# Performance work log

Hardware: AMD Instinct MI355X
Metric: run time of the kernel (lower is better)

Reference implementation:

```python
import math
import jax, jax.numpy as jnp
import numpy as np

B, S, D_MODEL = 4, 2048, 1024
N_HEADS, D_KV = 16, 64
INNER = N_HEADS * D_KV
NUM_BUCKETS = 32
MAX_DISTANCE = 128


def _relative_position_bucket(relative_position, bidirectional=True,
                              num_buckets=32, max_distance=128):
    # Faithful port of T5Attention._relative_position_bucket
    ret = jnp.zeros_like(relative_position)
    n = -relative_position
    if bidirectional:
        num_buckets //= 2
        ret = ret + (n < 0).astype(jnp.int32) * num_buckets
        n = jnp.abs(n)
    else:
        n = jnp.maximum(n, 0)
    max_exact = num_buckets // 2
    is_small = n < max_exact
    # safe log: n>=max_exact wherever this branch is selected
    val_if_large = max_exact + (
        jnp.log(jnp.maximum(n, 1).astype(jnp.float32) / max_exact)
        / math.log(max_distance / max_exact) * (num_buckets - max_exact)
    ).astype(jnp.int32)
    val_if_large = jnp.minimum(val_if_large, num_buckets - 1)
    return ret + jnp.where(is_small, n, val_if_large)


def setup_inputs() -> dict:
    key = jax.random.key(0)
    k_h, k_q, k_k, k_v, k_o, k_e = jax.random.split(key, 6)
    std = D_MODEL ** -0.5
    return {
        "hidden_states": jax.random.normal(k_h, (B, S, D_MODEL), dtype=jnp.float32),
        "Wq": jax.random.normal(k_q, (D_MODEL, INNER), dtype=jnp.float32) * std,
        "Wk": jax.random.normal(k_k, (D_MODEL, INNER), dtype=jnp.float32) * std,
        "Wv": jax.random.normal(k_v, (D_MODEL, INNER), dtype=jnp.float32) * std,
        "Wo": jax.random.normal(k_o, (INNER, D_MODEL), dtype=jnp.float32) * std,
        "rel_emb": jax.random.normal(k_e, (NUM_BUCKETS, N_HEADS), dtype=jnp.float32) * std,
    }


def reference(hidden_states, Wq, Wk, Wv, Wo, rel_emb):
    b, s, _ = hidden_states.shape
    # QKV projections (T5: no bias, no 1/sqrt(d) scaling of scores)
    def shape_heads(x):  # [b, s, inner] -> [b, h, s, d_kv]
        return x.reshape(b, s, N_HEADS, D_KV).transpose(0, 2, 1, 3)
    q = shape_heads(hidden_states @ Wq)
    k = shape_heads(hidden_states @ Wk)
    v = shape_heads(hidden_states @ Wv)

    scores = jnp.einsum("bhqd,bhkd->bhqk", q, k)  # [b, h, s, s]

    # relative position bias: sequential_relative_position + bucket + embed
    context_pos = jnp.arange(s, dtype=jnp.int32)[:, None]
    memory_pos = jnp.arange(s, dtype=jnp.int32)[None, :]
    rel_pos = memory_pos - context_pos  # [s, s]
    rp_bucket = _relative_position_bucket(rel_pos, bidirectional=True,
                                          num_buckets=NUM_BUCKETS,
                                          max_distance=MAX_DISTANCE)
    bias = rel_emb[rp_bucket]                       # [s, s, h]
    bias = bias.transpose(2, 0, 1)[None]            # [1, h, s, s]

    weights = jax.nn.softmax(scores + bias, axis=-1)
    context = jnp.einsum("bhqk,bhkd->bhqd", weights, v)
    context = context.transpose(0, 2, 1, 3).reshape(b, s, INNER)
    return context @ Wo
```

## Files before the change

### kernel.cpp

```cpp
#include <hip/hip_runtime.h>

typedef __bf16 bf16_t;
typedef __bf16 bf16x4 __attribute__((ext_vector_type(4)));
typedef __bf16 bf16x8 __attribute__((ext_vector_type(8)));
typedef float f32x4 __attribute__((ext_vector_type(4)));

#define NB 4
#define SS 2048
#define DM 1024
#define NH 16
#define DK 64
#define MM (NB*SS)
#define LOG2E 1.44269504f

__global__ __launch_bounds__(256) void k_prep(
    const float* __restrict__ H, bf16_t* __restrict__ Hbf,
    const float* __restrict__ W0, const float* __restrict__ W1,
    const float* __restrict__ W2, const float* __restrict__ W3,
    bf16_t* __restrict__ T0, bf16_t* __restrict__ T1,
    bf16_t* __restrict__ T2, bf16_t* __restrict__ T3,
    const float* __restrict__ rel_emb, float* __restrict__ biasT) {
  __shared__ float t[64][65];
  const int blk = blockIdx.x, tid = threadIdx.x;
  if (blk < 8192) {
    int i = blk * 256 + tid;
    float4 v = ((const float4*)H)[i];
    bf16x4 o = {(bf16_t)v.x, (bf16_t)v.y, (bf16_t)v.z, (bf16_t)v.w};
    *(bf16x4*)(Hbf + 4 * (size_t)i) = o;
  } else if (blk < 9216) {
    int tt = blk - 8192;
    int which = tt >> 8, rem = tt & 255;
    int k0 = (rem >> 4) * 64, n0 = (rem & 15) * 64;
    const float* W = which == 0 ? W0 : which == 1 ? W1 : which == 2 ? W2 : W3;
    bf16_t* T = which == 0 ? T0 : which == 1 ? T1 : which == 2 ? T2 : T3;
#pragma unroll
    for (int i = 0; i < 16; i++) {
      int idx = tid + i * 256; int r = idx >> 6, c = idx & 63;
      t[r][c] = W[(size_t)(k0 + r) * DM + n0 + c];
    }
    __syncthreads();
#pragma unroll
    for (int i = 0; i < 16; i++) {
      int idx = tid + i * 256; int r = idx >> 6, c = idx & 63;
      T[(size_t)(n0 + r) * DM + k0 + c] = (bf16_t)t[c][r];
    }
  } else {
    int tt = (blk - 9216) * 256 + tid;
    if (tt < 2 * SS - 1) {
      int rel = tt - (SS - 1);
      int n = -rel;
      int ret = 0;
      if (n < 0) { ret = 16; n = -n; }
      int bucket;
      if (n < 8) bucket = n;
      else {
        int v = 8 + (int)(logf((float)n * 0.125f) * (8.0f / logf(16.0f)));
        bucket = v < 15 ? v : 15;
      }
      bucket += ret;
#pragma unroll
      for (int h = 0; h < NH; h++)
        biasT[h * (2 * SS - 1) + tt] = rel_emb[bucket * NH + h] * LOG2E;
    }
  }
}

__device__ __forceinline__ void gld16(const bf16_t* g, bf16_t* l) {
  __builtin_amdgcn_global_load_lds(
      (const __attribute__((address_space(1))) unsigned int*)g,
      (__attribute__((address_space(3))) unsigned int*)l, 16, 0, 0);
}

__device__ __forceinline__ void gemm_tile(const bf16_t* __restrict__ A,
                                          const bf16_t* __restrict__ Bt, const int K,
                                          const int m0, const int n0,
                                          bf16_t* As, bf16_t* Bs, f32x4 (&acc)[4][4]) {
  const int tid = threadIdx.x;
  const int lane = tid & 63, wave = tid >> 6;
  const int l15 = lane & 15, quad = lane >> 4;
  const int wm = (wave >> 1) * 64, wn = (wave & 1) * 64;
  const int wwu = __builtin_amdgcn_readfirstlane(wave);
  const f32x4 z4 = {0.f, 0.f, 0.f, 0.f};
#pragma unroll
  for (int i = 0; i < 4; i++)
#pragma unroll
    for (int j = 0; j < 4; j++) acc[i][j] = z4;

  const int rr = lane >> 2;
  const int cc = (lane & 3) * 8;
  for (int k0 = 0; k0 < K; k0 += 32) {
    __syncthreads();
    gld16(A + (size_t)(m0 + wwu * 32 + rr) * K + k0 + cc,       As + wwu * 1024);
    gld16(A + (size_t)(m0 + wwu * 32 + 16 + rr) * K + k0 + cc,  As + wwu * 1024 + 512);
    gld16(Bt + (size_t)(n0 + wwu * 32 + rr) * K + k0 + cc,      Bs + wwu * 1024);
    gld16(Bt + (size_t)(n0 + wwu * 32 + 16 + rr) * K + k0 + cc, Bs + wwu * 1024 + 512);
    __syncthreads();
    bf16x8 af[4], bfr[4];
#pragma unroll
    for (int i = 0; i < 4; i++) {
      af[i]  = *(const bf16x8*)(As + (wm + i * 16 + l15) * 32 + quad * 8);
      bfr[i] = *(const bf16x8*)(Bs + (wn + i * 16 + l15) * 32 + quad * 8);
    }
#pragma unroll
    for (int i = 0; i < 4; i++)
#pragma unroll
      for (int j = 0; j < 4; j++)
        acc[i][j] = __builtin_amdgcn_mfma_f32_16x16x32_bf16(af[i], bfr[j], acc[i][j], 0, 0, 0);
  }
}

__global__ __launch_bounds__(256) void k_gemm_qkv(
    const bf16_t* __restrict__ A, const bf16_t* __restrict__ Wqt,
    const bf16_t* __restrict__ Wkt, const bf16_t* __restrict__ Wvt,
    bf16_t* __restrict__ Q, bf16_t* __restrict__ Kf, bf16_t* __restrict__ Vf) {
  __shared__ bf16_t As[128 * 32];
  __shared__ bf16_t Bs[128 * 32];
  const int which = blockIdx.z;
  const bf16_t* Bt = which == 0 ? Wqt : (which == 1 ? Wkt : Wvt);
  const int m0 = blockIdx.x * 128, n0 = blockIdx.y * 128;
  f32x4 acc[4][4];
  gemm_tile(A, Bt, DM, m0, n0, As, Bs, acc);

  const int tid = threadIdx.x;
  const int lane = tid & 63, wave = tid >> 6;
  const int l15 = lane & 15, quad = lane >> 4;
  const int wm = (wave >> 1) * 64, wn = (wave & 1) * 64;

  if (which == 0) {
#pragma unroll
    for (int i = 0; i < 4; i++)
#pragma unroll
      for (int j = 0; j < 4; j++)
#pragma unroll
        for (int r = 0; r < 4; r++) {
          int m = m0 + wm + i * 16 + quad * 4 + r;
          int n = n0 + wn + j * 16 + l15;
          int b = m >> 11, s = m & (SS - 1);
          int h = n >> 6, d = n & 63;
          Q[(((size_t)(b * NH + h)) * SS + s) * DK + d] = (bf16_t)(acc[i][j][r] * LOG2E);
        }
  } else if (which == 1) {
#pragma unroll
    for (int i = 0; i < 4; i++)
#pragma unroll
      for (int j = 0; j < 4; j++)
#pragma unroll
        for (int r = 0; r < 4; r++) {
          int m = m0 + wm + i * 16 + quad * 4 + r;
          int n = n0 + wn + j * 16 + l15;
          int b = m >> 11, s = m & (SS - 1);
          int h = n >> 6, d = n & 63;
          int slot = 4 * ((s >> 5) & 1) + 2 * ((s >> 2) & 1) + (d >> 5);
          int fl = ((d >> 3) & 3) * 16 + 4 * ((s >> 3) & 3) + (s & 3);
          Kf[(((size_t)(b * NH + h) * 32 + (s >> 6)) * 8 + slot) * 512 + fl * 8 + (d & 7)] =
              (bf16_t)acc[i][j][r];
        }
  } else {
#pragma unroll
    for (int i = 0; i < 4; i++)
#pragma unroll
      for (int j = 0; j < 4; j++) {
        int m = m0 + wm + i * 16 + quad * 4;
        int n = n0 + wn + j * 16 + l15;
        int b = m >> 11, s = m & (SS - 1);
        int h = n >> 6, d = n & 63;
        int slot = 4 * ((s >> 5) & 1) + (d >> 4);
        int fl = ((s >> 3) & 3) * 16 + (d & 15);
        bf16x4 pk = {(bf16_t)acc[i][j][0], (bf16_t)acc[i][j][1],
                     (bf16_t)acc[i][j][2], (bf16_t)acc[i][j][3]};
        *(bf16x4*)(&Vf[(((size_t)(b * NH + h) * 32 + (s >> 6)) * 8 + slot) * 512 +
                       fl * 8 + (s & 7)]) = pk;
      }
  }
}

__global__ __launch_bounds__(256, 2) void k_attn(const bf16_t* __restrict__ Qg,
                                                 const bf16_t* __restrict__ Kf,
                                                 const bf16_t* __restrict__ Vf,
                                                 const float* __restrict__ biasT,
                                                 bf16_t* __restrict__ ctx) {
  const int lin = blockIdx.x + 16 * blockIdx.y;
  const int nid = (lin & 7) * 128 + (lin >> 3);
  const int bh = nid >> 4;
  const int it0 = (nid & 15) * 128;
  const int b = bh >> 4, h = bh & 15;
  const bf16_t* Qp = Qg + ((size_t)bh * SS + it0) * DK;
  const float* biasH = biasT + h * (2 * SS - 1);

  __shared__ float bias2[512][2];
  __shared__ float OsumS[2][4][16];
  __shared__ f32x4 Ored[2 * 4 * 4 * 64];

  const int tid = threadIdx.x;
  const int lane = tid & 63, wave = tid >> 6;
  const int l15 = lane & 15, quad = lane >> 4;
  const int kh = wave & 1, qh = wave >> 1;

  for (int w = tid; w < 512; w += 256) {
    int g = w - 256 + (SS - 1);
    bias2[w][0] = biasH[g];
    bias2[w][1] = biasH[g + 1];
  }
  const float Bpos = biasH[(SS - 1) + 1024];
  const float Bneg = biasH[(SS - 1) - 1024];

  const bf16_t* KfB = Kf + (size_t)bh * 32 * 4096 + lane * 8;
  const bf16_t* VfB = Vf + (size_t)bh * 32 * 4096 + lane * 8;
  auto loadK = [&](int it, bf16x8 (&kf)[2][2]) {
    const bf16_t* kb = KfB + (size_t)it * 4096;
#pragma unroll
    for (int t = 0; t < 2; t++)
#pragma unroll
      for (int hf = 0; hf < 2; hf++)
        kf[t][hf] = *(const bf16x8*)(kb + ((2 * kh + t) * 2 + hf) * 512);
  };
  auto loadV = [&](int it, bf16x8 (&vf)[4]) {
    const bf16_t* vb = VfB + (size_t)it * 4096;
#pragma unroll
    for (int ni = 0; ni < 4; ni++)
      vf[ni] = *(const bf16x8*)(vb + (kh * 4 + ni) * 512);
  };

  bf16x8 qf[4][2];
#pragma unroll
  for (int mi = 0; mi < 4; mi++) {
    const bf16_t* qr = Qp + (size_t)(64 * qh + mi * 16 + l15) * DK + quad * 8;
    qf[mi][0] = *(const bf16x8*)qr;
    qf[mi][1] = *(const bf16x8*)(qr + 32);
  }

  f32x4 accO[4][4], accS[4];
  const f32x4 z4 = {0.f, 0.f, 0.f, 0.f};
#pragma unroll
  for (int mi = 0; mi < 4; mi++) {
    accS[mi] = z4;
#pragma unroll
    for (int ni = 0; ni < 4; ni++) accO[mi][ni] = z4;
  }
  const bf16_t one = (bf16_t)1.0f;
  const bf16x8 ones = {one, one, one, one, one, one, one, one};

  const int wb0 = 32 * kh + 8 * quad - 64 * qh - l15 - it0 + 256;

  auto step = [&](int it, bf16x8 (&kfC)[2][2], bf16x8 (&pfP)[4], bf16x8 (&vfP)[4],
                  bf16x8 (&pfC)[4]) {
    const int diff = it * 64 - it0;
    const bool band = (diff >= -128) && (diff < 256);
    const float cconst = diff >= 256 ? Bpos : Bneg;
    const f32x4 csplat = {cconst, cconst, cconst, cconst};
    const int jb = it * 64 + wb0;
#pragma unroll
    for (int mi = 0; mi < 4; mi++) {
      f32x4 c0, c1;
      if (band) {
        const int w = jb - mi * 16;
        float2 a0 = *(const float2*)bias2[w],     b0 = *(const float2*)bias2[w + 2];
        float2 a1 = *(const float2*)bias2[w + 4], b1 = *(const float2*)bias2[w + 6];
        c0 = f32x4{a0.x, a0.y, b0.x, b0.y};
        c1 = f32x4{a1.x, a1.y, b1.x, b1.y};
      } else {
        c0 = csplat;
        c1 = csplat;
      }
      f32x4 s0 = __builtin_amdgcn_mfma_f32_16x16x32_bf16(
          kfC[0][1], qf[mi][1],
          __builtin_amdgcn_mfma_f32_16x16x32_bf16(kfC[0][0], qf[mi][0], c0, 0, 0, 0), 0, 0, 0);
      f32x4 s1 = __builtin_amdgcn_mfma_f32_16x16x32_bf16(
          kfC[1][1], qf[mi][1],
          __builtin_amdgcn_mfma_f32_16x16x32_bf16(kfC[1][0], qf[mi][0], c1, 0, 0, 0), 0, 0, 0);
#pragma unroll
      for (int ni = 0; ni < 4; ni++)
        accO[mi][ni] =
            __builtin_amdgcn_mfma_f32_16x16x32_bf16(vfP[ni], pfP[mi], accO[mi][ni], 0, 0, 0);
      accS[mi] = __builtin_amdgcn_mfma_f32_16x16x32_bf16(ones, pfP[mi], accS[mi], 0, 0, 0);
      pfC[mi] =
          bf16x8{(bf16_t)__builtin_amdgcn_exp2f(s0[0]), (bf16_t)__builtin_amdgcn_exp2f(s0[1]),
                 (bf16_t)__builtin_amdgcn_exp2f(s0[2]), (bf16_t)__builtin_amdgcn_exp2f(s0[3]),
                 (bf16_t)__builtin_amdgcn_exp2f(s1[0]), (bf16_t)__builtin_amdgcn_exp2f(s1[1]),
                 (bf16_t)__builtin_amdgcn_exp2f(s1[2]), (bf16_t)__builtin_amdgcn_exp2f(s1[3])};
    }
  };
  auto step0 = [&](bf16x8 (&kfC)[2][2], bf16x8 (&pfC)[4]) {
    const int diff = -it0;
    const bool band = (diff >= -128) && (diff < 256);
    const float cconst = diff >= 256 ? Bpos : Bneg;
    const f32x4 csplat = {cconst, cconst, cconst, cconst};
    const int jb = wb0;
#pragma unroll
    for (int mi = 0; mi < 4; mi++) {
      f32x4 c0, c1;
      if (band) {
        const int w = jb - mi * 16;
        float2 a0 = *(const float2*)bias2[w],     b0 = *(const float2*)bias2[w + 2];
        float2 a1 = *(const float2*)bias2[w + 4], b1 = *(const float2*)bias2[w + 6];
        c0 = f32x4{a0.x, a0.y, b0.x, b0.y};
        c1 = f32x4{a1.x, a1.y, b1.x, b1.y};
      } else {
        c0 = csplat;
        c1 = csplat;
      }
      f32x4 s0 = __builtin_amdgcn_mfma_f32_16x16x32_bf16(
          kfC[0][1], qf[mi][1],
          __builtin_amdgcn_mfma_f32_16x16x32_bf16(kfC[0][0], qf[mi][0], c0, 0, 0, 0), 0, 0, 0);
      f32x4 s1 = __builtin_amdgcn_mfma_f32_16x16x32_bf16(
          kfC[1][1], qf[mi][1],
          __builtin_amdgcn_mfma_f32_16x16x32_bf16(kfC[1][0], qf[mi][0], c1, 0, 0, 0), 0, 0, 0);
      pfC[mi] =
          bf16x8{(bf16_t)__builtin_amdgcn_exp2f(s0[0]), (bf16_t)__builtin_amdgcn_exp2f(s0[1]),
                 (bf16_t)__builtin_amdgcn_exp2f(s0[2]), (bf16_t)__builtin_amdgcn_exp2f(s0[3]),
                 (bf16_t)__builtin_amdgcn_exp2f(s1[0]), (bf16_t)__builtin_amdgcn_exp2f(s1[1]),
                 (bf16_t)__builtin_amdgcn_exp2f(s1[2]), (bf16_t)__builtin_amdgcn_exp2f(s1[3])};
    }
  };

  bf16x8 kfA[2][2], vfA[4], kfB[2][2], vfB[4], pfA[4], pfB[4];
  loadK(0, kfA);
  loadV(0, vfA);
  __syncthreads();
  loadK(1, kfB);
  step0(kfA, pfA);
  loadV(1, vfB);

  for (int it = 1; it < 32; it += 2) {
    if (it + 1 < 32) loadK(it + 1, kfA);
    step(it, kfB, pfA, vfA, pfB);
    if (it + 1 < 32) {
      loadV(it + 1, vfA);
      loadK(it + 2, kfB);
      step(it + 1, kfA, pfB, vfB, pfA);
      loadV(it + 2, vfB);
    }
  }
#pragma unroll
  for (int mi = 0; mi < 4; mi++) {
#pragma unroll
    for (int ni = 0; ni < 4; ni++)
      accO[mi][ni] =
          __builtin_amdgcn_mfma_f32_16x16x32_bf16(vfB[ni], pfB[mi], accO[mi][ni], 0, 0, 0);
    accS[mi] = __builtin_amdgcn_mfma_f32_16x16x32_bf16(ones, pfB[mi], accS[mi], 0, 0, 0);
  }

  __syncthreads();
  if (kh) {
#pragma unroll
    for (int mi = 0; mi < 4; mi++) {
#pragma unroll
      for (int ni = 0; ni < 4; ni++)
        Ored[((qh * 4 + mi) * 4 + ni) * 64 + lane] = accO[mi][ni];
      if (quad == 0) OsumS[qh][mi][l15] = accS[mi][0];
    }
  }
  __syncthreads();
  if (!kh) {
#pragma unroll
    for (int mi = 0; mi < 4; mi++) {
      float l = accS[mi][0] + OsumS[qh][mi][l15];
      float inv = 1.0f / l;
      int srow = it0 + 64 * qh + mi * 16 + l15;
#pragma unroll
      for (int ni = 0; ni < 4; ni++) {
        f32x4 o = accO[mi][ni] + Ored[((qh * 4 + mi) * 4 + ni) * 64 + lane];
        bf16x4 pk = {(bf16_t)(o[0] * inv), (bf16_t)(o[1] * inv),
                     (bf16_t)(o[2] * inv), (bf16_t)(o[3] * inv)};
        *(bf16x4*)(&ctx[((size_t)(b * SS + srow)) * DM + h * DK + ni * 16 + quad * 4]) = pk;
      }
    }
  }
}

__global__ __launch_bounds__(256) void k_gemm_out(const bf16_t* __restrict__ A,
                                                  const bf16_t* __restrict__ Wot,
                                                  float* __restrict__ out) {
  __shared__ bf16_t As[128 * 32];
  __shared__ bf16_t Bs[128 * 32];
  const int m0 = blockIdx.x * 128, n0 = blockIdx.y * 128;
  f32x4 acc[4][4];
  gemm_tile(A, Wot, DM, m0, n0, As, Bs, acc);

  const int tid = threadIdx.x;
  const int lane = tid & 63, wave = tid >> 6;
  const int l15 = lane & 15, quad = lane >> 4;
  const int wm = (wave >> 1) * 64, wn = (wave & 1) * 64;
#pragma unroll
  for (int i = 0; i < 4; i++)
#pragma unroll
    for (int j = 0; j < 4; j++)
#pragma unroll
      for (int r = 0; r < 4; r++) {
        int m = m0 + wm + i * 16 + quad * 4 + r;
        int n = n0 + wn + j * 16 + l15;
        out[(size_t)m * DM + n] = acc[i][j][r];
      }
}

extern "C" void kernel_launch(void* const* d_in, const int* in_sizes, int n_in,
                              void* d_out, int out_size, void* d_ws, size_t ws_size,
                              hipStream_t stream) {
  (void)in_sizes; (void)n_in; (void)out_size; (void)ws_size;
  const float* H  = (const float*)d_in[0];
  const float* Wq = (const float*)d_in[1];
  const float* Wk = (const float*)d_in[2];
  const float* Wv = (const float*)d_in[3];
  const float* Wo = (const float*)d_in[4];
  const float* rel = (const float*)d_in[5];
  float* out = (float*)d_out;

  char* w = (char*)d_ws;
  bf16_t* Hbf = (bf16_t*)w; w += (size_t)MM * DM * 2;
  bf16_t* Wqt = (bf16_t*)w; w += (size_t)DM * DM * 2;
  bf16_t* Wkt = (bf16_t*)w; w += (size_t)DM * DM * 2;
  bf16_t* Wvt = (bf16_t*)w; w += (size_t)DM * DM * 2;
  bf16_t* Wot = (bf16_t*)w; w += (size_t)DM * DM * 2;
  bf16_t* Q   = (bf16_t*)w; w += (size_t)MM * DM * 2;
  bf16_t* Kf  = (bf16_t*)w; w += (size_t)MM * DM * 2;
  bf16_t* Vf  = (bf16_t*)w; w += (size_t)MM * DM * 2;
  bf16_t* CTX = (bf16_t*)w; w += (size_t)MM * DM * 2;
  float* biasT = (float*)w;

  k_prep<<<9232, 256, 0, stream>>>(H, Hbf, Wq, Wk, Wv, Wo, Wqt, Wkt, Wvt, Wot, rel, biasT);
  k_gemm_qkv<<<dim3(MM / 128, DM / 128, 3), 256, 0, stream>>>(Hbf, Wqt, Wkt, Wvt, Q, Kf, Vf);
  k_attn<<<dim3(SS / 128, NB * NH), 256, 0, stream>>>(Q, Kf, Vf, biasT, CTX);
  k_gemm_out<<<dim3(MM / 128, DM / 128), 256, 0, stream>>>(CTX, Wot, out);
}
```

Measured before the change: 260.7 us.

## Replace QKV GEMM with 256x256-tile pipelined kernel over fused QKV weights

Replaces the 128x128 QKV projection GEMM with a 512-thread kernel that computes 256x256 tiles over one concatenated 3072-column weight matrix. It uses swizzled, double-buffered LDS staging through global_load_lds, split into fine-grained phases with explicit vmcnt waits, barriers and MFMA priority boosts. Block ids are remapped so neighbouring tiles run on the same XCD. The goal is more data reuse per LDS load and hiding global-load latency behind the matrix math. The cost is higher LDS and register use, which limits occupancy to one block per CU. It also relies on Wqt, Wkt and Wvt sitting contiguously in the workspace.

```diff
diff --git a/kernel.cpp b/kernel.cpp
--- a/kernel.cpp
+++ b/kernel.cpp
@@ -71,6 +71,162 @@
       (__attribute__((address_space(3))) unsigned int*)l, 16, 0, 0);
 }
 
+#define VMC(n) asm volatile("s_waitcnt vmcnt(" #n ")" ::: "memory")
+#define SBAR() do { __builtin_amdgcn_sched_barrier(0); __builtin_amdgcn_s_barrier(); } while (0)
+
+__device__ __forceinline__ void gemm256(const bf16_t* __restrict__ A,
+                                        const bf16_t* __restrict__ Bt,
+                                        const int m0, const int n0,
+                                        bf16_t* ldsA, bf16_t* ldsB,
+                                        f32x4 (&acc)[8][4]) {
+  const int tid = threadIdx.x;
+  const int lane = tid & 63, l15 = lane & 15, quad = lane >> 4;
+  const int wave = tid >> 6;
+  const int wvu = __builtin_amdgcn_readfirstlane(wave);
+  const int wm2 = wave >> 2, wn4 = wave & 3;
+  const f32x4 z4 = {0.f, 0.f, 0.f, 0.f};
+#pragma unroll
+  for (int i = 0; i < 8; i++)
+#pragma unroll
+    for (int j = 0; j < 4; j++) acc[i][j] = z4;
+
+  auto stage = [&](const bf16_t* G, int gr0, int k0, bf16_t* dstbase) {
+#pragma unroll
+    for (int j = 0; j < 2; j++) {
+      const int L = wvu * 2048 + j * 1024 + lane * 16;
+      const int row = L >> 7;
+      const int colb = (L & 127) ^ ((row & 7) << 4);
+      gld16(G + (size_t)(gr0 + row) * DM + k0 + (colb >> 1),
+            dstbase + ((wvu * 2048 + j * 1024) >> 1));
+    }
+  };
+
+#define STGA(tt, hf, bb) if ((tt) < 16) stage(A, m0 + (hf) * 128, (tt) * 64, \
+                                              ldsA + ((bb) * 2 + (hf)) * 8192)
+#define STGB(tt, hf, bb) if ((tt) < 16) stage(Bt, n0 + (hf) * 128, (tt) * 64, \
+                                              ldsB + ((bb) * 2 + (hf)) * 8192)
+
+  STGA(0, 0, 0); STGA(0, 1, 0); STGB(0, 0, 0); STGB(0, 1, 0); STGA(1, 0, 1);
+  VMC(2);
+  SBAR();
+
+#define PHASE(bb, mh, nh, STG_STMT, VMSTMT)                                              \
+  {                                                                                      \
+    bf16x8 af[4][2], bfr[2][2];                                                          \
+    _Pragma("unroll") for (int mi = 0; mi < 4; mi++)                                     \
+    _Pragma("unroll") for (int kk = 0; kk < 2; kk++) {                                   \
+      const int ml = wm2 * 128 + (mh) * 64 + mi * 16 + l15;                              \
+      const int row = ml & 127;                                                          \
+      const int cb = (kk * 64 + quad * 16) ^ ((row & 7) << 4);                           \
+      af[mi][kk] = *(const bf16x8*)(ldsA + ((bb) * 2 + (ml >> 7)) * 8192 +               \
+                                    row * 64 + (cb >> 1));                               \
+    }                                                                                    \
+    _Pragma("unroll") for (int ni = 0; ni < 2; ni++)                                     \
+    _Pragma("unroll") for (int kk = 0; kk < 2; kk++) {                                   \
+      const int nl = wn4 * 64 + (nh) * 32 + ni * 16 + l15;                               \
+      const int row = nl & 127;                                                          \
+      const int cb = (kk * 64 + quad * 16) ^ ((row & 7) << 4);                           \
+      bfr[ni][kk] = *(const bf16x8*)(ldsB + ((bb) * 2 + (nl >> 7)) * 8192 +              \
+                                     row * 64 + (cb >> 1));                              \
+    }                                                                                    \
+    STG_STMT;                                                                            \
+    SBAR();                                                                              \
+    __builtin_amdgcn_s_setprio(1);                                                       \
+    _Pragma("unroll") for (int mi = 0; mi < 4; mi++)                                     \
+    _Pragma("unroll") for (int ni = 0; ni < 2; ni++) {                                   \
+      acc[(mh) * 4 + mi][(nh) * 2 + ni] = __builtin_amdgcn_mfma_f32_16x16x32_bf16(       \
+          af[mi][0], bfr[ni][0], acc[(mh) * 4 + mi][(nh) * 2 + ni], 0, 0, 0);            \
+      acc[(mh) * 4 + mi][(nh) * 2 + ni] = __builtin_amdgcn_mfma_f32_16x16x32_bf16(       \
+          af[mi][1], bfr[ni][1], acc[(mh) * 4 + mi][(nh) * 2 + ni], 0, 0, 0);            \
+    }                                                                                    \
+    __builtin_amdgcn_s_setprio(0);                                                       \
+    VMSTMT;                                                                              \
+    SBAR();                                                                              \
+  }
+
+  for (int it2 = 0; it2 < 8; ++it2) {
+    const int t = 2 * it2;
+    PHASE(0, 0, 0, STGB(t + 1, 0, 1), );
+    PHASE(0, 0, 1, STGB(t + 1, 1, 1), VMC(6));
+    PHASE(0, 1, 0, STGA(t + 1, 1, 1), );
+    PHASE(0, 1, 1, STGA(t + 2, 0, 0), VMC(4));
+    PHASE(1, 0, 0, STGB(t + 2, 0, 0), );
+    PHASE(1, 0, 1, STGB(t + 2, 1, 0), VMC(6));
+    PHASE(1, 1, 0, STGA(t + 2, 1, 0), );
+    PHASE(1, 1, 1, STGA(t + 3, 0, 1), VMC(4));
+  }
+#undef PHASE
+#undef STGA
+#undef STGB
+}
+
+__global__ __launch_bounds__(512, 1) void k_gemm_qkv(
+    const bf16_t* __restrict__ A, const bf16_t* __restrict__ Wt,
+    bf16_t* __restrict__ Q, bf16_t* __restrict__ Kf, bf16_t* __restrict__ Vf) {
+  __shared__ bf16_t ldsA[4 * 8192];
+  __shared__ bf16_t ldsB[4 * 8192];
+  const int lin = blockIdx.x;
+  const int id = (lin & 7) * 48 + (lin >> 3);
+  const int np = id >> 5, mp = id & 31;
+  const int m0 = mp * 256, n0 = np * 256;
+  f32x4 acc[8][4];
+  gemm256(A, Wt, m0, n0, ldsA, ldsB, acc);
+
+  const int tid = threadIdx.x;
+  const int lane = tid & 63, l15 = lane & 15, quad = lane >> 4;
+  const int wave = tid >> 6;
+  const int wm = (wave >> 2) * 128, wn = (wave & 3) * 64;
+  const int ng = n0 + wn;
+  const int which = ng >> 10;
+  const int h = (ng & 1023) >> 6;
+  const int mb = m0 + wm;
+  const int b = mb >> 11;
+  const int sb = mb & (SS - 1);
+
+  if (which == 0) {
+#pragma unroll
+    for (int ig = 0; ig < 8; ig++)
+#pragma unroll
+      for (int jg = 0; jg < 4; jg++) {
+        const int d = jg * 16 + l15;
+#pragma unroll
+        for (int r = 0; r < 4; r++) {
+          const int s = sb + ig * 16 + quad * 4 + r;
+          Q[(((size_t)(b * NH + h)) * SS + s) * DK + d] = (bf16_t)(acc[ig][jg][r] * LOG2E);
+        }
+      }
+  } else if (which == 1) {
+#pragma unroll
+    for (int ig = 0; ig < 8; ig++)
+#pragma unroll
+      for (int jg = 0; jg < 4; jg++) {
+        const int d = jg * 16 + l15;
+#pragma unroll
+        for (int r = 0; r < 4; r++) {
+          const int s = sb + ig * 16 + quad * 4 + r;
+          const int slot = 4 * ((s >> 5) & 1) + 2 * ((s >> 2) & 1) + (d >> 5);
+          const int fl = ((d >> 3) & 3) * 16 + 4 * ((s >> 3) & 3) + (s & 3);
+          Kf[(((size_t)(b * NH + h) * 32 + (s >> 6)) * 8 + slot) * 512 + fl * 8 + (d & 7)] =
+              (bf16_t)acc[ig][jg][r];
+        }
+      }
+  } else {
+#pragma unroll
+    for (int ig = 0; ig < 8; ig++)
+#pragma unroll
+      for (int jg = 0; jg < 4; jg++) {
+        const int s = sb + ig * 16 + quad * 4;
+        const int d = jg * 16 + l15;
+        const int slot = 4 * ((s >> 5) & 1) + (d >> 4);
+        const int fl = ((s >> 3) & 3) * 16 + (d & 15);
+        bf16x4 pk = {(bf16_t)acc[ig][jg][0], (bf16_t)acc[ig][jg][1],
+                     (bf16_t)acc[ig][jg][2], (bf16_t)acc[ig][jg][3]};
+        *(bf16x4*)(&Vf[(((size_t)(b * NH + h) * 32 + (s >> 6)) * 8 + slot) * 512 +
+                       fl * 8 + (s & 7)]) = pk;
+      }
+  }
+}
+
 __device__ __forceinline__ void gemm_tile(const bf16_t* __restrict__ A,
                                           const bf16_t* __restrict__ Bt, const int K,
                                           const int m0, const int n0,
@@ -106,71 +262,6 @@
 #pragma unroll
       for (int j = 0; j < 4; j++)
         acc[i][j] = __builtin_amdgcn_mfma_f32_16x16x32_bf16(af[i], bfr[j], acc[i][j], 0, 0, 0);
-  }
-}
-
-__global__ __launch_bounds__(256) void k_gemm_qkv(
-    const bf16_t* __restrict__ A, const bf16_t* __restrict__ Wqt,
-    const bf16_t* __restrict__ Wkt, const bf16_t* __restrict__ Wvt,
-    bf16_t* __restrict__ Q, bf16_t* __restrict__ Kf, bf16_t* __restrict__ Vf) {
-  __shared__ bf16_t As[128 * 32];
-  __shared__ bf16_t Bs[128 * 32];
-  const int which = blockIdx.z;
-  const bf16_t* Bt = which == 0 ? Wqt : (which == 1 ? Wkt : Wvt);
-  const int m0 = blockIdx.x * 128, n0 = blockIdx.y * 128;
-  f32x4 acc[4][4];
-  gemm_tile(A, Bt, DM, m0, n0, As, Bs, acc);
-
-  const int tid = threadIdx.x;
-  const int lane = tid & 63, wave = tid >> 6;
-  const int l15 = lane & 15, quad = lane >> 4;
-  const int wm = (wave >> 1) * 64, wn = (wave & 1) * 64;
-
-  if (which == 0) {
-#pragma unroll
-    for (int i = 0; i < 4; i++)
-#pragma unroll
-      for (int j = 0; j < 4; j++)
-#pragma unroll
-        for (int r = 0; r < 4; r++) {
-          int m = m0 + wm + i * 16 + quad * 4 + r;
-          int n = n0 + wn + j * 16 + l15;
-          int b = m >> 11, s = m & (SS - 1);
-          int h = n >> 6, d = n & 63;
-          Q[(((size_t)(b * NH + h)) * SS + s) * DK + d] = (bf16_t)(acc[i][j][r] * LOG2E);
-        }
-  } else if (which == 1) {
-#pragma unroll
-    for (int i = 0; i < 4; i++)
-#pragma unroll
-      for (int j = 0; j < 4; j++)
-#pragma unroll
-        for (int r = 0; r < 4; r++) {
-          int m = m0 + wm + i * 16 + quad * 4 + r;
-          int n = n0 + wn + j * 16 + l15;
-          int b = m >> 11, s = m & (SS - 1);
-          int h = n >> 6, d = n & 63;
-          int slot = 4 * ((s >> 5) & 1) + 2 * ((s >> 2) & 1) + (d >> 5);
-          int fl = ((d >> 3) & 3) * 16 + 4 * ((s >> 3) & 3) + (s & 3);
-          Kf[(((size_t)(b * NH + h) * 32 + (s >> 6)) * 8 + slot) * 512 + fl * 8 + (d & 7)] =
-              (bf16_t)acc[i][j][r];
-        }
-  } else {
-#pragma unroll
-    for (int i = 0; i < 4; i++)
-#pragma unroll
-      for (int j = 0; j < 4; j++) {
-        int m = m0 + wm + i * 16 + quad * 4;
-        int n = n0 + wn + j * 16 + l15;
-        int b = m >> 11, s = m & (SS - 1);
-        int h = n >> 6, d = n & 63;
-        int slot = 4 * ((s >> 5) & 1) + (d >> 4);
-        int fl = ((s >> 3) & 3) * 16 + (d & 15);
-        bf16x4 pk = {(bf16_t)acc[i][j][0], (bf16_t)acc[i][j][1],
-                     (bf16_t)acc[i][j][2], (bf16_t)acc[i][j][3]};
-        *(bf16x4*)(&Vf[(((size_t)(b * NH + h) * 32 + (s >> 6)) * 8 + slot) * 512 +
-                       fl * 8 + (s & 7)]) = pk;
-      }
   }
 }
 
@@ -418,7 +509,7 @@
   float* biasT = (float*)w;
 
   k_prep<<<9232, 256, 0, stream>>>(H, Hbf, Wq, Wk, Wv, Wo, Wqt, Wkt, Wvt, Wot, rel, biasT);
-  k_gemm_qkv<<<dim3(MM / 128, DM / 128, 3), 256, 0, stream>>>(Hbf, Wqt, Wkt, Wvt, Q, Kf, Vf);
+  k_gemm_qkv<<<384, 512, 0, stream>>>(Hbf, Wqt, Q, Kf, Vf);
   k_attn<<<dim3(SS / 128, NB * NH), 256, 0, stream>>>(Q, Kf, Vf, biasT, CTX);
   k_gemm_out<<<dim3(MM / 128, DM / 128), 256, 0, stream>>>(CTX, Wot, out);
 }
```

Result: slower. 281.6 us (+8.0%).

## Pre-fragment QKV weights and load B operands directly into registers

Applied to the files above, without the earlier changes.

The prep kernel now writes the transposed Q/K/V weights in an MFMA-fragment-ordered layout (fidx), so each lane can load its B operand straight from global memory into registers. This drops the B shared-memory tile from the QKV GEMM. The main loop is rewritten as a manually scheduled, register-double-buffered pipeline with direct-to-LDS A loads, explicit waitcnt and barriers. It cuts LDS traffic and bank pressure for B, but it relies on hand-placed waits and sched barriers and shares one A buffer across half-steps, which constrains overlap.

```diff
diff --git a/kernel.cpp b/kernel.cpp
--- a/kernel.cpp
+++ b/kernel.cpp
@@ -12,6 +12,13 @@
 #define DK 64
 #define MM (NB*SS)
 #define LOG2E 1.44269504f
+
+#define VMC(n) asm volatile("s_waitcnt vmcnt(" #n ")" ::: "memory")
+#define LGKM0() asm volatile("s_waitcnt lgkmcnt(0)" ::: "memory")
+
+__device__ __forceinline__ int fidx(int n, int k) {
+  return ((n >> 4) * 32 + (k >> 5)) * 512 + ((n & 15) + ((k >> 3) & 3) * 16) * 8 + (k & 7);
+}
 
 __global__ __launch_bounds__(256) void k_prep(
     const float* __restrict__ H, bf16_t* __restrict__ Hbf,
@@ -39,10 +46,18 @@
       t[r][c] = W[(size_t)(k0 + r) * DM + n0 + c];
     }
     __syncthreads();
-#pragma unroll
-    for (int i = 0; i < 16; i++) {
-      int idx = tid + i * 256; int r = idx >> 6, c = idx & 63;
-      T[(size_t)(n0 + r) * DM + k0 + c] = (bf16_t)t[c][r];
+    if (which < 3) {
+#pragma unroll
+      for (int i = 0; i < 16; i++) {
+        int idx = tid + i * 256; int r = idx >> 6, c = idx & 63;
+        T[fidx(n0 + r, k0 + c)] = (bf16_t)t[c][r];
+      }
+    } else {
+#pragma unroll
+      for (int i = 0; i < 16; i++) {
+        int idx = tid + i * 256; int r = idx >> 6, c = idx & 63;
+        T[(size_t)(n0 + r) * DM + k0 + c] = (bf16_t)t[c][r];
+      }
     }
   } else {
     int tt = (blk - 9216) * 256 + tid;
@@ -114,17 +129,82 @@
     const bf16_t* __restrict__ Wkt, const bf16_t* __restrict__ Wvt,
     bf16_t* __restrict__ Q, bf16_t* __restrict__ Kf, bf16_t* __restrict__ Vf) {
   __shared__ bf16_t As[128 * 32];
-  __shared__ bf16_t Bs[128 * 32];
   const int which = blockIdx.z;
-  const bf16_t* Bt = which == 0 ? Wqt : (which == 1 ? Wkt : Wvt);
+  const bf16_t* Bf = which == 0 ? Wqt : (which == 1 ? Wkt : Wvt);
   const int m0 = blockIdx.x * 128, n0 = blockIdx.y * 128;
-  f32x4 acc[4][4];
-  gemm_tile(A, Bt, DM, m0, n0, As, Bs, acc);
-
   const int tid = threadIdx.x;
   const int lane = tid & 63, wave = tid >> 6;
   const int l15 = lane & 15, quad = lane >> 4;
   const int wm = (wave >> 1) * 64, wn = (wave & 1) * 64;
+  const int wwu = __builtin_amdgcn_readfirstlane(wave);
+  const int rr = lane >> 2, cc = (lane & 3) * 8;
+
+  const bf16_t* Bb = Bf + ((n0 + wn) >> 4) * 16384 + lane * 8;
+  const bf16_t* Arow0 = A + (size_t)(m0 + wwu * 32 + rr) * DM + cc;
+  const bf16_t* Arow1 = Arow0 + (size_t)16 * DM;
+
+  f32x4 acc[4][4];
+  const f32x4 z4 = {0.f, 0.f, 0.f, 0.f};
+#pragma unroll
+  for (int i = 0; i < 4; i++)
+#pragma unroll
+    for (int j = 0; j < 4; j++) acc[i][j] = z4;
+
+  bf16x8 bc[4], bn[4];
+#pragma unroll
+  for (int j = 0; j < 4; j++) bc[j] = *(const bf16x8*)(Bb + j * 16384);
+
+  for (int it2 = 0; it2 < 16; ++it2) {
+    const int t = 2 * it2;
+    LGKM0();
+    __builtin_amdgcn_sched_barrier(0);
+    __builtin_amdgcn_s_barrier();
+    gld16(Arow0 + t * 32, As + wwu * 1024);
+    gld16(Arow1 + t * 32, As + wwu * 1024 + 512);
+    __builtin_amdgcn_sched_barrier(0);
+#pragma unroll
+    for (int j = 0; j < 4; j++) bn[j] = *(const bf16x8*)(Bb + j * 16384 + (t + 1) * 512);
+    VMC(4);
+    __builtin_amdgcn_sched_barrier(0);
+    __builtin_amdgcn_s_barrier();
+    {
+      bf16x8 af[4];
+#pragma unroll
+      for (int i = 0; i < 4; i++)
+        af[i] = *(const bf16x8*)(As + (wm + i * 16 + l15) * 32 + quad * 8);
+#pragma unroll
+      for (int i = 0; i < 4; i++)
+#pragma unroll
+        for (int j = 0; j < 4; j++)
+          acc[i][j] = __builtin_amdgcn_mfma_f32_16x16x32_bf16(af[i], bc[j], acc[i][j], 0, 0, 0);
+    }
+    LGKM0();
+    __builtin_amdgcn_sched_barrier(0);
+    __builtin_amdgcn_s_barrier();
+    gld16(Arow0 + (t + 1) * 32, As + wwu * 1024);
+    gld16(Arow1 + (t + 1) * 32, As + wwu * 1024 + 512);
+    __builtin_amdgcn_sched_barrier(0);
+    if (it2 < 15) {
+#pragma unroll
+      for (int j = 0; j < 4; j++) bc[j] = *(const bf16x8*)(Bb + j * 16384 + (t + 2) * 512);
+      VMC(4);
+    } else {
+      VMC(0);
+    }
+    __builtin_amdgcn_sched_barrier(0);
+    __builtin_amdgcn_s_barrier();
+    {
+      bf16x8 af[4];
+#pragma unroll
+      for (int i = 0; i < 4; i++)
+        af[i] = *(const bf16x8*)(As + (wm + i * 16 + l15) * 32 + quad * 8);
+#pragma unroll
+      for (int i = 0; i < 4; i++)
+#pragma unroll
+        for (int j = 0; j < 4; j++)
+          acc[i][j] = __builtin_amdgcn_mfma_f32_16x16x32_bf16(af[i], bn[j], acc[i][j], 0, 0, 0);
+    }
+  }
 
   if (which == 0) {
 #pragma unroll
```

After: 262.0 us. Within noise of the previous version (+0.5%).
